# Performance work log

Hardware: AMD Instinct MI355X
Metric: run time of the kernel (lower is better)

## Reference

```python
import jax, jax.numpy as jnp
import numpy as np

B, L, D = 64, 128, 768          # batch, padded seq len, bert dim
H, HA = 1024, 256               # d_label_hidden, d_label_hidden_arc
POS, V = 18, 40                 # pos vocab, arc (deprel) vocab


def setup_inputs() -> dict:
    key = jax.random.key(0)
    ks = jax.random.split(key, 24)
    n = lambda i, shape, s=0.02: jax.random.normal(ks[i], shape, jnp.float32) * s
    # realistic padding: random sentence lengths in [L//2, L]
    lengths = jax.random.randint(ks[1], (B,), L // 2, L + 1)
    pad_mask = (jnp.arange(L)[None, :] < lengths[:, None]).astype(jnp.float32)
    heads = jax.random.randint(ks[2], (B, L), 0, L)
    # mark padded positions as -1 (zero head vector), as in the original loop
    heads = jnp.where(pad_mask > 0, heads, -1)
    return {
        "ann": jax.random.normal(ks[0], (B, L, D), jnp.float32),
        "pad_mask": pad_mask,
        "correct_heads": heads,
        # label-biaffine branch (hidden H)
        "W_head_mlp": n(3, (D, H)), "b_head_mlp": n(4, (H,)),
        "W_dep_mlp": n(5, (D, H)), "b_dep_mlp": n(6, (H,)),
        "W_lin": n(7, (H, H)), "b_lin": n(8, (H,)),
        "head_vec": n(9, (H,), 1.0), "dep_vec": n(10, (H,), 1.0),
        "bias": n(11, (1, 1, 1), 1.0),
        # arc-label biaffine branch (hidden HA, per-label bilinear)
        "W_head_arc_mlp": n(12, (D, HA)), "b_head_arc_mlp": n(13, (HA,)),
        "W_dep_arc_mlp": n(14, (D, HA)), "b_dep_arc_mlp": n(15, (HA,)),
        "W_arc": n(16, (V, HA, HA), 1.0),
        "head_vec_arc": n(17, (HA, V), 1.0), "dep_vec_arc": n(18, (HA, V), 1.0),
        "bias_arc": n(19, (1, 1, V), 1.0),
        # POS tip
        "W_pos": n(20, (D, POS)), "b_pos": n(21, (POS,)),
    }


def reference(ann, pad_mask, correct_heads,
              W_head_mlp, b_head_mlp, W_dep_mlp, b_dep_mlp,
              W_lin, b_lin, head_vec, dep_vec, bias,
              W_head_arc_mlp, b_head_arc_mlp, W_dep_arc_mlp, b_dep_arc_mlp,
              W_arc, head_vec_arc, dep_vec_arc, bias_arc,
              W_pos, b_pos):
    # POS prediction
    pos_pred = ann @ W_pos + b_pos                                  # [B,L,POS]

    # ---- dependency (unlabeled arc) biaffine ----
    ann_head = jax.nn.relu(ann @ W_head_mlp + b_head_mlp)           # [B,L,H]
    ann_dep = jax.nn.relu(ann @ W_dep_mlp + b_dep_mlp)              # [B,L,H]
    head_bias = ann_head @ head_vec                                 # [B,L]
    dep_bias = ann_dep @ dep_vec                                    # [B,L]
    Wh = ann_head @ W_lin + b_lin                                   # [B,L,H]
    # scores[b,i,j] = dep[b,i] . Wh[b,j]
    dep_W_headT = jnp.einsum('bih,bjh->bij', ann_dep, Wh)
    dep_W_headT = dep_W_headT + head_bias[:, None, :] + dep_bias[:, :, None] + bias
    valid_head = pad_mask[:, None, :] > 0                           # [B,1,L]
    dep_W_headT = jnp.where(valid_head, dep_W_headT, -jnp.inf)

    # ---- labeled arc biaffine (gather gold head per dependent) ----
    ann_head_arc = jax.nn.relu(ann @ W_head_arc_mlp + b_head_arc_mlp)  # [B,L,HA]
    ann_dep_arc = jax.nn.relu(ann @ W_dep_arc_mlp + b_dep_arc_mlp)     # [B,L,HA]
    idx = jnp.clip(correct_heads, 0, L - 1)
    gathered = jnp.take_along_axis(ann_head_arc, idx[:, :, None], axis=1)
    gathered = jnp.where((correct_heads == -1)[:, :, None], 0.0, gathered)  # [B,L,HA]

    head_arc_bias = gathered @ head_vec_arc                         # [B,L,V]
    dep_arc_bias = ann_dep_arc @ dep_vec_arc                        # [B,L,V]
    # per-label bilinear: s[b,l,v] = gathered[b,l] . W_arc[v] . dep[b,l]
    dep_W_headT_arc = jnp.einsum('bld,vde,ble->blv', gathered, W_arc, ann_dep_arc)
    dep_W_headT_arc = dep_W_headT_arc + head_arc_bias + dep_arc_bias + bias_arc

    return pos_pred, dep_W_headT, dep_W_headT_arc
```

## Files before the change

### kernel.cpp

```cpp
#include <hip/hip_runtime.h>
#include <hip/hip_bf16.h>

#define B_ 64
#define L_ 128
#define D_ 768
#define H_ 1024
#define HA_ 256
#define POS_ 18
#define V_ 40
#define BL_ (B_ * L_)

#define NEG_BIG (-1.0e30f)

typedef __attribute__((ext_vector_type(8))) short short8v;
typedef __attribute__((ext_vector_type(4))) short short4v;
typedef __attribute__((ext_vector_type(4))) float f32x4;

__device__ inline void split_bf16(float x, short& hi, short& lo) {
  __hip_bfloat16 h = __float2bfloat16(x);
  hi = *reinterpret_cast<short*>(&h);
  const float r = x - __bfloat162float(h);
  __hip_bfloat16 l = __float2bfloat16(r);
  lo = *reinterpret_cast<short*>(&l);
}

__device__ __forceinline__ short f2b(float x) {
  __hip_bfloat16 h = __float2bfloat16(x);
  return *reinterpret_cast<short*>(&h);
}
__device__ __forceinline__ float b2f(short s) {
  __hip_bfloat16 h = *reinterpret_cast<__hip_bfloat16*>(&s);
  return __bfloat162float(h);
}

__device__ __forceinline__ int swz8(int row, int s) { return ((s + (row >> 1)) & 3) * 8; }
__device__ __forceinline__ int colswz(int row, int n) {
  return (n & ~31) + swz8(row, (n >> 3) & 3) + (n & 7);
}

__device__ __forceinline__ void ld_lds16(const void* g, void* l) {
  __builtin_amdgcn_global_load_lds(
      (const __attribute__((address_space(1))) unsigned int*)g,
      (__attribute__((address_space(3))) unsigned int*)l, 16, 0, 0);
}

template<bool RELU, bool HASBIAS>
__global__ __launch_bounds__(256)
void gemm_bias(const float* __restrict__ A, const float* __restrict__ Bm,
               const float* __restrict__ bias, float* __restrict__ C,
               int M, int N, int K) {
  __shared__ __align__(16) float As[16][68];
  __shared__ __align__(16) float Bs[16][68];
  const int t = threadIdx.x;
  const int tx = t & 15, ty = t >> 4;
  const int m0 = blockIdx.y * 64, n0 = blockIdx.x * 64;
  const int arow = t >> 2, aks = (t & 3) * 4;
  const int bkr = t >> 4, bns = (t & 15) * 4;
  float acc[4][4] = {};
  for (int k0 = 0; k0 < K; k0 += 16) {
    const float4 av = *reinterpret_cast<const float4*>(&A[(size_t)(m0 + arow) * K + k0 + aks]);
    float4 bv;
    const int nb = n0 + bns;
    if (nb + 3 < N) {
      bv = *reinterpret_cast<const float4*>(&Bm[(size_t)(k0 + bkr) * N + nb]);
    } else {
      bv.x = (nb + 0 < N) ? Bm[(size_t)(k0 + bkr) * N + nb + 0] : 0.f;
      bv.y = (nb + 1 < N) ? Bm[(size_t)(k0 + bkr) * N + nb + 1] : 0.f;
      bv.z = (nb + 2 < N) ? Bm[(size_t)(k0 + bkr) * N + nb + 2] : 0.f;
      bv.w = 0.f;
    }
    __syncthreads();
    As[aks + 0][arow] = av.x;
    As[aks + 1][arow] = av.y;
    As[aks + 2][arow] = av.z;
    As[aks + 3][arow] = av.w;
    *reinterpret_cast<float4*>(&Bs[bkr][bns]) = bv;
    __syncthreads();
#pragma unroll
    for (int kk = 0; kk < 16; ++kk) {
      const float4 a4 = *reinterpret_cast<const float4*>(&As[kk][ty * 4]);
      const float4 b4 = *reinterpret_cast<const float4*>(&Bs[kk][tx * 4]);
      const float aa[4] = {a4.x, a4.y, a4.z, a4.w};
      const float bb[4] = {b4.x, b4.y, b4.z, b4.w};
#pragma unroll
      for (int i = 0; i < 4; ++i)
#pragma unroll
        for (int j = 0; j < 4; ++j)
          acc[i][j] = fmaf(aa[i], bb[j], acc[i][j]);
    }
  }
#pragma unroll
  for (int j = 0; j < 4; ++j) {
    const int n = n0 + tx * 4 + j;
    if (n >= N) continue;
    float bj = 0.f;
    if constexpr (HASBIAS) bj = bias[n];
#pragma unroll
    for (int i = 0; i < 4; ++i) {
      const int m = m0 + ty * 4 + i;
      float v = acc[i][j] + bj;
      if (RELU) v = fmaxf(v, 0.f);
      C[(size_t)m * N + n] = v;
    }
  }
}

__global__ __launch_bounds__(256)
void split_pre(const float* __restrict__ src, short* __restrict__ hi,
               short* __restrict__ lo, int K) {
  const int t = threadIdx.x;
  const int r = blockIdx.x * 4 + (t >> 6);
  const int lane = t & 63;
  for (int c = lane * 4; c < K; c += 256) {
    const float4 v = *reinterpret_cast<const float4*>(&src[(size_t)r * K + c]);
    const float vv[4] = {v.x, v.y, v.z, v.w};
    short4v h4, l4;
#pragma unroll
    for (int j = 0; j < 4; ++j) {
      short h, l;
      split_bf16(vv[j], h, l);
      h4[j] = h; l4[j] = l;
    }
    const int cs = colswz(r, c);
    *reinterpret_cast<short4v*>(&hi[(size_t)r * K + cs]) = h4;
    *reinterpret_cast<short4v*>(&lo[(size_t)r * K + cs]) = l4;
  }
}

__global__ __launch_bounds__(256)
void transpose_h(const float* __restrict__ W, short* __restrict__ Thi,
                 int K, int N) {
  __shared__ float tile[32][33];
  const int k0 = blockIdx.y * 32, n0 = blockIdx.x * 32;
  const int t = threadIdx.x;
  const int r = t >> 3, c = (t & 7) * 4;
  const float4 w4 = *reinterpret_cast<const float4*>(&W[(size_t)(k0 + r) * N + n0 + c]);
  tile[r][c + 0] = w4.x;
  tile[r][c + 1] = w4.y;
  tile[r][c + 2] = w4.z;
  tile[r][c + 3] = w4.w;
  __syncthreads();
  short4v hi4;
#pragma unroll
  for (int j = 0; j < 4; ++j) hi4[j] = f2b(tile[c + j][r]);
  const int row = n0 + r;
  const int cs = swz8(row, (c >> 3) & 3) + (c & 7);
  *reinterpret_cast<short4v*>(&Thi[(size_t)row * K + k0 + cs]) = hi4;
}

__global__ __launch_bounds__(256)
void transpose_pos(const float* __restrict__ W, short* __restrict__ Th,
                   short* __restrict__ Tl) {
  const int t = threadIdx.x;
  const int k0 = blockIdx.x * 32;
  const int n = t & 31;
  const int ks = (t >> 5) * 4;
#pragma unroll
  for (int j = 0; j < 4; ++j) {
    const int k = k0 + ks + j;
    const float v = (n < POS_) ? W[(size_t)k * POS_ + n] : 0.f;
    short h, l;
    split_bf16(v, h, l);
    Th[(size_t)n * D_ + colswz(n, k)] = h;
    Tl[(size_t)n * D_ + colswz(n, k)] = l;
  }
}

#define GEMM_H_BODY                                                           \
  __shared__ __align__(16) short AhP[2][4096];                                \
  __shared__ __align__(16) short BhP[2][4096];                                \
  const int t = threadIdx.x;                                                  \
  const int lane = t & 63, w = t >> 6;                                        \
  const int wm = w >> 1, wn = w & 1;                                          \
  const int m0 = blockIdx.y * 128, n0 = blockIdx.x * 128;                     \
  const int fr = lane & 15, kgi = lane >> 4;                                  \
  const int drow = lane >> 2, dslot = lane & 3;                               \
  f32x4 acc[4][4] = {};                                                       \
  const int nt = K >> 5;                                                      \
  auto stage = [&](int tt, int pb) {                  \
    const int k0 = tt << 5;                                                   \
    _Pragma("unroll")                                                         \
    for (int cc = 0; cc < 2; ++cc) {                                          \
      const int c = w * 2 + cc;                                               \
      const size_t ga = (size_t)(m0 + c * 16 + drow) * K + k0 + dslot * 8;    \
      ld_lds16(&Ath[ga], &AhP[pb][c * 512]);                                  \
      const size_t gb = (size_t)(n0 + c * 16 + drow) * K + k0 + dslot * 8;    \
      ld_lds16(&Bth[gb], &BhP[pb][c * 512]);                                  \
    }                                                                         \
  };                                                                          \
  auto compute = [&](int pb) {                                                \
    short8v ah[4];                                                            \
    _Pragma("unroll")                                                         \
    for (int mi = 0; mi < 4; ++mi) {                                          \
      const int r = wm * 64 + mi * 16 + fr;                                   \
      ah[mi] = *reinterpret_cast<const short8v*>(&AhP[pb][r * 32 + swz8(r, kgi)]); \
    }                                                                         \
    __builtin_amdgcn_s_setprio(1);                                            \
    _Pragma("unroll")                                                         \
    for (int nj = 0; nj < 4; ++nj) {                                          \
      const int rn = wn * 64 + nj * 16 + fr;                                  \
      const short8v bh = *reinterpret_cast<const short8v*>(&BhP[pb][rn * 32 + swz8(rn, kgi)]); \
      _Pragma("unroll")                                                       \
      for (int mi = 0; mi < 4; ++mi)                                          \
        acc[mi][nj] = __builtin_amdgcn_mfma_f32_16x16x32_bf16(ah[mi], bh, acc[mi][nj], 0, 0, 0); \
    }                                                                         \
    __builtin_amdgcn_s_setprio(0);                                            \
  };                                                                          \
  stage(0, 0);                                                                \
  int cur = 0;                                                                \
  for (int tt = 0; tt < nt; ++tt) {                                           \
    if (tt + 1 < nt) {                                                        \
      stage(tt + 1, cur ^ 1);                                                 \
      asm volatile("s_waitcnt vmcnt(4)" ::: "memory");                        \
    } else {                                                                  \
      asm volatile("s_waitcnt vmcnt(0)" ::: "memory");                        \
    }                                                                         \
    __builtin_amdgcn_s_barrier();                                             \
    compute(cur);                                                             \
    __builtin_amdgcn_s_barrier();                                             \
    cur ^= 1;                                                                 \
  }                                                                           \
  const int rg = lane >> 4;

template<bool RELU>
__global__ __launch_bounds__(256)
void gemm_h(const short* __restrict__ Ath, const short* __restrict__ Bth,
            const float* __restrict__ bias, float* __restrict__ C,
            int M, int N, int K) {
  GEMM_H_BODY
#pragma unroll
  for (int nj = 0; nj < 4; ++nj) {
    const int n = n0 + wn * 64 + nj * 16 + fr;
    const float bj = bias[n];
#pragma unroll
    for (int mi = 0; mi < 4; ++mi) {
#pragma unroll
      for (int q = 0; q < 4; ++q) {
        const int m = m0 + wm * 64 + mi * 16 + rg * 4 + q;
        float v2 = acc[mi][nj][q] + bj;
        if (RELU) v2 = fmaxf(v2, 0.f);
        C[(size_t)m * N + n] = v2;
      }
    }
  }
}

template<bool RELU>
__global__ __launch_bounds__(256)
void gemm_hs(const short* __restrict__ Ath, const short* __restrict__ Bth,
             const float* __restrict__ bias, short* __restrict__ Oh,
             int M, int N, int K) {
  GEMM_H_BODY
#pragma unroll
  for (int nj = 0; nj < 4; ++nj) {
    const int n = n0 + wn * 64 + nj * 16 + fr;
    const float bj = bias[n];
#pragma unroll
    for (int mi = 0; mi < 4; ++mi) {
#pragma unroll
      for (int q = 0; q < 4; ++q) {
        const int m = m0 + wm * 64 + mi * 16 + rg * 4 + q;
        float v2 = acc[mi][nj][q] + bj;
        if (RELU) v2 = fmaxf(v2, 0.f);
        Oh[(size_t)m * N + colswz(m, n)] = f2b(v2);
      }
    }
  }
}

__global__ __launch_bounds__(256)
void pos_mfma(const short* __restrict__ Ath, const short* __restrict__ Atl,
              const short* __restrict__ Pth, const short* __restrict__ Ptl,
              const float* __restrict__ bias, float* __restrict__ out) {
  extern __shared__ short sm[];
  short* AhP = sm;
  short* AlP = sm + 16384;
  short* BhP = sm + 32768;
  short* BlP = sm + 34816;
  const int t = threadIdx.x;
  const int m0 = blockIdx.x * 256;
  const int lane = t & 63, w = t >> 6;
  const int fr = lane & 15, kgi = lane >> 4;
  const int drow = lane >> 2, dslot = lane & 3;
  f32x4 acc[4][2] = {};

  auto stage = [&](int tt, int pb) {
    const int k0 = tt << 5;
#pragma unroll
    for (int cc = 0; cc < 4; ++cc) {
      const int c = w * 4 + cc;
      const size_t ga = (size_t)(m0 + c * 16 + drow) * D_ + k0 + dslot * 8;
      ld_lds16(&Ath[ga], &AhP[pb * 8192 + c * 512]);
      ld_lds16(&Atl[ga], &AlP[pb * 8192 + c * 512]);
    }
    {
      const short* bsrc = (w & 2) ? Ptl : Pth;
      short* bdst = (w & 2) ? BlP : BhP;
      const int c = w & 1;
      const size_t gb = (size_t)(c * 16 + drow) * D_ + k0 + dslot * 8;
      ld_lds16(&bsrc[gb], &bdst[pb * 1024 + c * 512]);
    }
  };
  auto compute = [&](int pb) {
    short8v ah[4], al[4];
#pragma unroll
    for (int mi = 0; mi < 4; ++mi) {
      const int r = w * 64 + mi * 16 + fr;
      const int sw = swz8(r, kgi);
      ah[mi] = *reinterpret_cast<const short8v*>(&AhP[pb * 8192 + r * 32 + sw]);
      al[mi] = *reinterpret_cast<const short8v*>(&AlP[pb * 8192 + r * 32 + sw]);
    }
#pragma unroll
    for (int nj = 0; nj < 2; ++nj) {
      const int rn = nj * 16 + fr;
      const int sw = swz8(rn, kgi);
      const short8v bh = *reinterpret_cast<const short8v*>(&BhP[pb * 1024 + rn * 32 + sw]);
      const short8v bl = *reinterpret_cast<const short8v*>(&BlP[pb * 1024 + rn * 32 + sw]);
#pragma unroll
      for (int mi = 0; mi < 4; ++mi) {
        acc[mi][nj] = __builtin_amdgcn_mfma_f32_16x16x32_bf16(ah[mi], bh, acc[mi][nj], 0, 0, 0);
        acc[mi][nj] = __builtin_amdgcn_mfma_f32_16x16x32_bf16(al[mi], bh, acc[mi][nj], 0, 0, 0);
        acc[mi][nj] = __builtin_amdgcn_mfma_f32_16x16x32_bf16(ah[mi], bl, acc[mi][nj], 0, 0, 0);
      }
    }
  };

  stage(0, 0);
  __syncthreads();
  int cur = 0;
  for (int tt = 0; tt < 24; ++tt) {
    if (tt + 1 < 24) stage(tt + 1, cur ^ 1);
    compute(cur);
    __syncthreads();
    cur ^= 1;
  }

  const int rg = lane >> 4;
#pragma unroll
  for (int nj = 0; nj < 2; ++nj) {
    const int n = nj * 16 + fr;
    if (n >= POS_) continue;
    const float bj = bias[n];
#pragma unroll
    for (int mi = 0; mi < 4; ++mi) {
#pragma unroll
      for (int q = 0; q < 4; ++q) {
        const int m = m0 + w * 64 + mi * 16 + rg * 4 + q;
        out[(size_t)m * POS_ + n] = acc[mi][nj][q] + bj;
      }
    }
  }
}

__global__ __launch_bounds__(256)
void bias_dots_h(const short* __restrict__ Ahh, const short* __restrict__ Adh,
                 const float* __restrict__ head_vec, const float* __restrict__ dep_vec,
                 float* __restrict__ hb, float* __restrict__ db) {
  const int m = blockIdx.x;
  const int t = threadIdx.x;
  const int c = t * 4;
  const size_t o = (size_t)m * H_ + colswz(m, c);
  const short4v h4 = *reinterpret_cast<const short4v*>(&Ahh[o]);
  const short4v d4 = *reinterpret_cast<const short4v*>(&Adh[o]);
  const float4 hv = *reinterpret_cast<const float4*>(&head_vec[c]);
  const float4 dv = *reinterpret_cast<const float4*>(&dep_vec[c]);
  const float hvv[4] = {hv.x, hv.y, hv.z, hv.w};
  const float dvv[4] = {dv.x, dv.y, dv.z, dv.w};
  float sh = 0.f, sd = 0.f;
#pragma unroll
  for (int j = 0; j < 4; ++j) {
    sh = fmaf(b2f(h4[j]), hvv[j], sh);
    sd = fmaf(b2f(d4[j]), dvv[j], sd);
  }
#pragma unroll
  for (int off = 32; off; off >>= 1) {
    sh += __shfl_xor(sh, off);
    sd += __shfl_xor(sd, off);
  }
  __shared__ float redh[4], redd[4];
  const int w = t >> 6;
  if ((t & 63) == 0) { redh[w] = sh; redd[w] = sd; }
  __syncthreads();
  if (t == 0) {
    hb[m] = redh[0] + redh[1] + redh[2] + redh[3];
    db[m] = redd[0] + redd[1] + redd[2] + redd[3];
  }
}

__global__ __launch_bounds__(256)
void scores_h(const short* __restrict__ Adh, const short* __restrict__ Whh,
              const float* __restrict__ hb, const float* __restrict__ db,
              const float* __restrict__ pad_mask, const float* __restrict__ bias1,
              float* __restrict__ out2) {
  __shared__ __align__(16) short AhP[2][2048];
  __shared__ __align__(16) short BhP[2][2048];
  const int t = threadIdx.x;
  const int b = blockIdx.z;
  const int i0 = blockIdx.y * 64, j0 = blockIdx.x * 64;
  const int lane = t & 63, w = t >> 6;
  const int wm = w >> 1, wn = w & 1;
  const int fr = lane & 15, kgi = lane >> 4;
  const int drow = lane >> 2, dslot = lane & 3;
  const size_t abase = ((size_t)b * L_ + i0) * H_;
  const size_t bbase = ((size_t)b * L_ + j0) * H_;
  f32x4 acc[2][2] = {};

  auto stage = [&](int tt, int pb) {
    const int k0 = tt << 5;
    const size_t ga = abase + (size_t)(w * 16 + drow) * H_ + k0 + dslot * 8;
    ld_lds16(&Adh[ga], &AhP[pb][w * 512]);
    const size_t gb = bbase + (size_t)(w * 16 + drow) * H_ + k0 + dslot * 8;
    ld_lds16(&Whh[gb], &BhP[pb][w * 512]);
  };
  auto compute = [&](int pb) {
    short8v ah[2];
#pragma unroll
    for (int mi = 0; mi < 2; ++mi) {
      const int r = wm * 32 + mi * 16 + fr;
      ah[mi] = *reinterpret_cast<const short8v*>(&AhP[pb][r * 32 + swz8(r, kgi)]);
    }
    __builtin_amdgcn_s_setprio(1);
#pragma unroll
    for (int nj = 0; nj < 2; ++nj) {
      const int rn = wn * 32 + nj * 16 + fr;
      const short8v bh = *reinterpret_cast<const short8v*>(&BhP[pb][rn * 32 + swz8(rn, kgi)]);
#pragma unroll
      for (int mi = 0; mi < 2; ++mi)
        acc[mi][nj] = __builtin_amdgcn_mfma_f32_16x16x32_bf16(ah[mi], bh, acc[mi][nj], 0, 0, 0);
    }
    __builtin_amdgcn_s_setprio(0);
  };

  stage(0, 0);
  int cur = 0;
  for (int tt = 0; tt < 32; ++tt) {
    if (tt + 1 < 32) {
      stage(tt + 1, cur ^ 1);
      asm volatile("s_waitcnt vmcnt(2)" ::: "memory");
    } else {
      asm volatile("s_waitcnt vmcnt(0)" ::: "memory");
    }
    __builtin_amdgcn_s_barrier();
    compute(cur);
    __builtin_amdgcn_s_barrier();
    cur ^= 1;
  }

  const int rg = lane >> 4;
  const float bias0 = bias1[0];
#pragma unroll
  for (int nj = 0; nj < 2; ++nj) {
    const int jcol = j0 + wn * 32 + nj * 16 + fr;
    const float mj = pad_mask[b * L_ + jcol];
    const float hbj = hb[b * L_ + jcol];
#pragma unroll
    for (int mi = 0; mi < 2; ++mi) {
#pragma unroll
      for (int q = 0; q < 4; ++q) {
        const int irow = i0 + wm * 32 + mi * 16 + rg * 4 + q;
        float v = acc[mi][nj][q] + hbj + db[b * L_ + irow] + bias0;
        if (!(mj > 0.f)) v = NEG_BIG;
        out2[((size_t)b * L_ + irow) * L_ + jcol] = v;
      }
    }
  }
}

__global__ __launch_bounds__(256)
void transposeW_h(const float* __restrict__ W, short* __restrict__ Whi) {
  __shared__ float tile[32][33];
  const int v = blockIdx.z, d0 = blockIdx.y * 32, e0 = blockIdx.x * 32;
  const int t = threadIdx.x;
  const int r = t >> 3, c = (t & 7) * 4;
  const float4 w4 = *reinterpret_cast<const float4*>(
      &W[((size_t)v * HA_ + d0 + r) * HA_ + e0 + c]);
  tile[r][c + 0] = w4.x;
  tile[r][c + 1] = w4.y;
  tile[r][c + 2] = w4.z;
  tile[r][c + 3] = w4.w;
  __syncthreads();
  short4v hi4;
#pragma unroll
  for (int j = 0; j < 4; ++j) hi4[j] = f2b(tile[c + j][r]);
  const int row = e0 + r;
  const int cs = swz8(row, (c >> 3) & 3) + (c & 7);
  *reinterpret_cast<short4v*>(&Whi[((size_t)v * HA_ + row) * HA_ + d0 + cs]) = hi4;
}

__global__ __launch_bounds__(256)
void gather_h(const float* __restrict__ head_arcb, const int* __restrict__ heads,
              float* __restrict__ g32, short* __restrict__ g_hi) {
  const int t = threadIdx.x;
  const int m = blockIdx.x * 4 + (t >> 6);
  const int lane = t & 63;
  const int h = heads[m];
  float4 g4 = make_float4(0.f, 0.f, 0.f, 0.f);
  if (h >= 0)
    g4 = *reinterpret_cast<const float4*>(
        &head_arcb[((size_t)((m >> 7) * L_ + h)) * HA_ + lane * 4]);
  *reinterpret_cast<float4*>(&g32[(size_t)m * HA_ + lane * 4]) = g4;
  short4v hi4;
  const float gv[4] = {g4.x, g4.y, g4.z, g4.w};
#pragma unroll
  for (int j = 0; j < 4; ++j) hi4[j] = f2b(gv[j]);
  *reinterpret_cast<short4v*>(&g_hi[(size_t)m * HA_ + colswz(m, lane * 4)]) = hi4;
}

__global__ __launch_bounds__(512)
void arc_h(const short* __restrict__ g_hi, const short* __restrict__ Wt_hi,
           const float* __restrict__ dep32, const float* __restrict__ hb_arc,
           const float* __restrict__ db_arc, float* __restrict__ out3) {
  extern __shared__ short sm[];
  short* AhP = sm;
  short* BhP = sm + 16384;
  __shared__ float parts[256][2];
  const int t = threadIdx.x;
  const int bid = blockIdx.x;
  const int xcd = bid & 7;
  const int j = bid >> 3;
  const int m0 = (j / 5) * 256;
  const int v = xcd * 5 + (j % 5);
  const int lane = t & 63, w = t >> 6;
  const int wm = w >> 1, we = w & 1;
  const int fr = lane & 15, kgi = lane >> 4;
  const int drow = lane >> 2, dslot = lane & 3;
  const size_t wbase = (size_t)v * HA_ * HA_;

  f32x4 acc[4][8] = {};

  auto stage = [&](int tt, int pb) {
    const int k0 = tt << 5;
#pragma unroll
    for (int cc = 0; cc < 2; ++cc) {
      const int c = w * 2 + cc;
      const size_t ga = (size_t)(m0 + c * 16 + drow) * HA_ + k0 + dslot * 8;
      ld_lds16(&g_hi[ga], &AhP[pb * 8192 + c * 512]);
      const size_t gb = wbase + (size_t)(c * 16 + drow) * HA_ + k0 + dslot * 8;
      ld_lds16(&Wt_hi[gb], &BhP[pb * 8192 + c * 512]);
    }
  };
  auto compute = [&](int pb) {
    short8v ah[4];
#pragma unroll
    for (int mi = 0; mi < 4; ++mi) {
      const int r = wm * 64 + mi * 16 + fr;
      ah[mi] = *reinterpret_cast<const short8v*>(&AhP[pb * 8192 + r * 32 + swz8(r, kgi)]);
    }
    __builtin_amdgcn_s_setprio(1);
#pragma unroll
    for (int ej = 0; ej < 8; ++ej) {
      const int rb = we * 128 + ej * 16 + fr;
      const short8v bh = *reinterpret_cast<const short8v*>(&BhP[pb * 8192 + rb * 32 + swz8(rb, kgi)]);
#pragma unroll
      for (int mi = 0; mi < 4; ++mi)
        acc[mi][ej] = __builtin_amdgcn_mfma_f32_16x16x32_bf16(ah[mi], bh, acc[mi][ej], 0, 0, 0);
    }
    __builtin_amdgcn_s_setprio(0);
  };

  stage(0, 0);
  int cur = 0;
#pragma unroll
  for (int tt = 0; tt < 8; ++tt) {
    if (tt < 7) {
      stage(tt + 1, cur ^ 1);
      asm volatile("s_waitcnt vmcnt(4)" ::: "memory");
    } else {
      asm volatile("s_waitcnt vmcnt(0)" ::: "memory");
    }
    __builtin_amdgcn_s_barrier();
    compute(cur);
    __builtin_amdgcn_s_barrier();
    cur ^= 1;
  }

  const int rg = lane >> 4;
#pragma unroll
  for (int mi = 0; mi < 4; ++mi) {
#pragma unroll
    for (int q = 0; q < 4; ++q) {
      const int mrow = wm * 64 + mi * 16 + rg * 4 + q;
      const int m = m0 + mrow;
      float s = 0.f;
#pragma unroll
      for (int ej = 0; ej < 8; ++ej)
        s = fmaf(acc[mi][ej][q], dep32[(size_t)m * HA_ + we * 128 + ej * 16 + fr], s);
      s += __shfl_xor(s, 1, 16);
      s += __shfl_xor(s, 2, 16);
      s += __shfl_xor(s, 4, 16);
      s += __shfl_xor(s, 8, 16);
      if (fr == 0) parts[mrow][we] = s;
    }
  }
  __syncthreads();
  if (t < 256) {
    const int m = m0 + t;
    out3[(size_t)m * V_ + v] =
        parts[t][0] + parts[t][1] + hb_arc[(size_t)m * V_ + v] + db_arc[(size_t)m * V_ + v];
  }
}

extern "C" void kernel_launch(void* const* d_in, const int* in_sizes, int n_in,
                              void* d_out, int out_size, void* d_ws, size_t ws_size,
                              hipStream_t stream) {
  const float* ann        = (const float*)d_in[0];
  const float* pad_mask   = (const float*)d_in[1];
  const int*   heads      = (const int*)d_in[2];
  const float* W_head_mlp = (const float*)d_in[3];
  const float* b_head_mlp = (const float*)d_in[4];
  const float* W_dep_mlp  = (const float*)d_in[5];
  const float* b_dep_mlp  = (const float*)d_in[6];
  const float* W_lin      = (const float*)d_in[7];
  const float* b_lin      = (const float*)d_in[8];
  const float* head_vec   = (const float*)d_in[9];
  const float* dep_vec    = (const float*)d_in[10];
  const float* bias1      = (const float*)d_in[11];
  const float* W_head_arc = (const float*)d_in[12];
  const float* b_head_arc = (const float*)d_in[13];
  const float* W_dep_arc  = (const float*)d_in[14];
  const float* b_dep_arc  = (const float*)d_in[15];
  const float* W_arc      = (const float*)d_in[16];
  const float* hv_arc     = (const float*)d_in[17];
  const float* dv_arc     = (const float*)d_in[18];
  const float* bias_arc   = (const float*)d_in[19];
  const float* W_pos      = (const float*)d_in[20];
  const float* b_pos      = (const float*)d_in[21];

  float* out_pos    = (float*)d_out;
  float* out_scores = out_pos + (size_t)BL_ * POS_;
  float* out_arc    = out_scores + (size_t)B_ * L_ * L_;

  float* ws  = (float*)d_ws;
  float* R1  = ws;
  float* R2  = R1 + (size_t)BL_ * H_;
  float* R3  = R2 + (size_t)BL_ * H_;
  float* head_arcb = R3 + (size_t)BL_ * H_;
  float* dep_arcb  = head_arcb + (size_t)BL_ * HA_;
  float* hb        = dep_arcb + (size_t)BL_ * HA_;
  float* db        = hb + BL_;
  short* wt0     = (short*)(db + BL_);
  short* Wth_hm  = wt0;
  short* Wth_dm  = Wth_hm + (size_t)H_ * D_;
  short* Wth_lin = Wth_dm + (size_t)H_ * D_;
  short* Wth_ha  = Wth_lin + (size_t)H_ * H_;
  short* Wth_da  = Wth_ha + (size_t)HA_ * D_;
  short* Pth     = Wth_da + (size_t)HA_ * D_;
  short* Ptl     = Pth + (size_t)32 * D_;
  short* Ahh = (short*)R1;
  short* Adh = (short*)R2;
  short* Ath = (short*)R3;  short* Atl = Ath + (size_t)BL_ * D_;
  short* Whh = (short*)R3;
  float* g32 = (float*)wt0;
  short* Wt_hi  = (short*)R1;
  short* g_hi   = Wt_hi + (size_t)V_ * HA_ * HA_;
  float* hb_arc = (float*)(g_hi + (size_t)BL_ * HA_);
  float* db_arc = hb_arc + (size_t)BL_ * V_;

  {
    hipFuncSetAttribute((const void*)pos_mfma, hipFuncAttributeMaxDynamicSharedMemorySize, 73728);
    hipFuncSetAttribute((const void*)arc_h, hipFuncAttributeMaxDynamicSharedMemorySize, 65536);
  }

  const dim3 blk(256);
  split_pre<<<dim3(BL_ / 4), blk, 0, stream>>>(ann, Ath, Atl, D_);
  transpose_h<<<dim3(H_ / 32, D_ / 32), blk, 0, stream>>>(W_head_mlp, Wth_hm, D_, H_);
  transpose_h<<<dim3(H_ / 32, D_ / 32), blk, 0, stream>>>(W_dep_mlp, Wth_dm, D_, H_);
  transpose_h<<<dim3(H_ / 32, H_ / 32), blk, 0, stream>>>(W_lin, Wth_lin, H_, H_);
  transpose_h<<<dim3(HA_ / 32, D_ / 32), blk, 0, stream>>>(W_head_arc, Wth_ha, D_, HA_);
  transpose_h<<<dim3(HA_ / 32, D_ / 32), blk, 0, stream>>>(W_dep_arc, Wth_da, D_, HA_);
  transpose_pos<<<dim3(D_ / 32), blk, 0, stream>>>(W_pos, Pth, Ptl);

  gemm_hs<true><<<dim3(H_ / 128, BL_ / 128), blk, 0, stream>>>(
      Ath, Wth_hm, b_head_mlp, Ahh, BL_, H_, D_);
  gemm_hs<true><<<dim3(H_ / 128, BL_ / 128), blk, 0, stream>>>(
      Ath, Wth_dm, b_dep_mlp, Adh, BL_, H_, D_);
  gemm_h<true><<<dim3(HA_ / 128, BL_ / 128), blk, 0, stream>>>(
      Ath, Wth_ha, b_head_arc, head_arcb, BL_, HA_, D_);
  gemm_h<true><<<dim3(HA_ / 128, BL_ / 128), blk, 0, stream>>>(
      Ath, Wth_da, b_dep_arc, dep_arcb, BL_, HA_, D_);
  pos_mfma<<<dim3(BL_ / 256), blk, 73728, stream>>>(Ath, Atl, Pth, Ptl, b_pos, out_pos);
  gemm_hs<false><<<dim3(H_ / 128, BL_ / 128), blk, 0, stream>>>(
      Ahh, Wth_lin, b_lin, Whh, BL_, H_, H_);

  bias_dots_h<<<dim3(BL_), blk, 0, stream>>>(Ahh, Adh, head_vec, dep_vec, hb, db);
  scores_h<<<dim3(2, 2, B_), blk, 0, stream>>>(
      Adh, Whh, hb, db, pad_mask, bias1, out_scores);

  transposeW_h<<<dim3(HA_ / 32, HA_ / 32, V_), blk, 0, stream>>>(W_arc, Wt_hi);
  gather_h<<<dim3(BL_ / 4), blk, 0, stream>>>(head_arcb, heads, g32, g_hi);
  gemm_bias<false, true><<<dim3(1, BL_ / 64), blk, 0, stream>>>(
      g32, hv_arc, bias_arc, hb_arc, BL_, V_, HA_);
  gemm_bias<false, false><<<dim3(1, BL_ / 64), blk, 0, stream>>>(
      dep_arcb, dv_arc, nullptr, db_arc, BL_, V_, HA_);
  arc_h<<<dim3((BL_ / 256) * V_), dim3(512), 65536, stream>>>(
      g_hi, Wt_hi, dep_arcb, hb_arc, db_arc, out_arc);
}
```

Before: 302.0 us.

## Fuse dep-arc bias into arc kernel, retile arc_h, restructure bias dots and pos sync

The dep_arc_bias GEMM is folded into the arc bilinear kernel: dv_arc[e,v] is added to each accumulator before the dot with the dep vector, which removes one launch and the db_arc round trip. arc_h drops from 512 to 256 threads with 128-row tiles and static LDS, doubling the grid. bias_dots_h now computes one row per wavefront with no shared-memory reduction, and pos_mfma replaces __syncthreads with explicit vmcnt waits plus raw barriers. The vmcnt counts are hand-tuned and depend on how many loads each stage issues.

```diff
diff --git a/kernel.cpp b/kernel.cpp
--- a/kernel.cpp
+++ b/kernel.cpp
@@ -326,12 +326,17 @@
   };
 
   stage(0, 0);
-  __syncthreads();
   int cur = 0;
   for (int tt = 0; tt < 24; ++tt) {
-    if (tt + 1 < 24) stage(tt + 1, cur ^ 1);
+    if (tt + 1 < 24) {
+      stage(tt + 1, cur ^ 1);
+      asm volatile("s_waitcnt vmcnt(9)" ::: "memory");
+    } else {
+      asm volatile("s_waitcnt vmcnt(0)" ::: "memory");
+    }
+    __builtin_amdgcn_s_barrier();
     compute(cur);
-    __syncthreads();
+    __builtin_amdgcn_s_barrier();
     cur ^= 1;
   }
 
@@ -356,34 +361,34 @@
 void bias_dots_h(const short* __restrict__ Ahh, const short* __restrict__ Adh,
                  const float* __restrict__ head_vec, const float* __restrict__ dep_vec,
                  float* __restrict__ hb, float* __restrict__ db) {
-  const int m = blockIdx.x;
-  const int t = threadIdx.x;
-  const int c = t * 4;
-  const size_t o = (size_t)m * H_ + colswz(m, c);
-  const short4v h4 = *reinterpret_cast<const short4v*>(&Ahh[o]);
-  const short4v d4 = *reinterpret_cast<const short4v*>(&Adh[o]);
-  const float4 hv = *reinterpret_cast<const float4*>(&head_vec[c]);
-  const float4 dv = *reinterpret_cast<const float4*>(&dep_vec[c]);
-  const float hvv[4] = {hv.x, hv.y, hv.z, hv.w};
-  const float dvv[4] = {dv.x, dv.y, dv.z, dv.w};
+  const int t = threadIdx.x;
+  const int m = blockIdx.x * 4 + (t >> 6);
+  const int lane = t & 63;
   float sh = 0.f, sd = 0.f;
 #pragma unroll
-  for (int j = 0; j < 4; ++j) {
-    sh = fmaf(b2f(h4[j]), hvv[j], sh);
-    sd = fmaf(b2f(d4[j]), dvv[j], sd);
+  for (int jj = 0; jj < 4; ++jj) {
+    const int c = lane * 16 + jj * 4;
+    const size_t o = (size_t)m * H_ + colswz(m, c);
+    const short4v h4 = *reinterpret_cast<const short4v*>(&Ahh[o]);
+    const short4v d4 = *reinterpret_cast<const short4v*>(&Adh[o]);
+    const float4 hv = *reinterpret_cast<const float4*>(&head_vec[c]);
+    const float4 dv = *reinterpret_cast<const float4*>(&dep_vec[c]);
+    const float hvv[4] = {hv.x, hv.y, hv.z, hv.w};
+    const float dvv[4] = {dv.x, dv.y, dv.z, dv.w};
+#pragma unroll
+    for (int j = 0; j < 4; ++j) {
+      sh = fmaf(b2f(h4[j]), hvv[j], sh);
+      sd = fmaf(b2f(d4[j]), dvv[j], sd);
+    }
   }
 #pragma unroll
   for (int off = 32; off; off >>= 1) {
     sh += __shfl_xor(sh, off);
     sd += __shfl_xor(sd, off);
   }
-  __shared__ float redh[4], redd[4];
-  const int w = t >> 6;
-  if ((t & 63) == 0) { redh[w] = sh; redd[w] = sd; }
-  __syncthreads();
-  if (t == 0) {
-    hb[m] = redh[0] + redh[1] + redh[2] + redh[3];
-    db[m] = redd[0] + redd[1] + redd[2] + redd[3];
+  if (lane == 0) {
+    hb[m] = sh;
+    db[m] = sd;
   }
 }
 
@@ -506,19 +511,18 @@
   *reinterpret_cast<short4v*>(&g_hi[(size_t)m * HA_ + colswz(m, lane * 4)]) = hi4;
 }
 
-__global__ __launch_bounds__(512)
+__global__ __launch_bounds__(256)
 void arc_h(const short* __restrict__ g_hi, const short* __restrict__ Wt_hi,
            const float* __restrict__ dep32, const float* __restrict__ hb_arc,
-           const float* __restrict__ db_arc, float* __restrict__ out3) {
-  extern __shared__ short sm[];
-  short* AhP = sm;
-  short* BhP = sm + 16384;
-  __shared__ float parts[256][2];
+           const float* __restrict__ dv_arc, float* __restrict__ out3) {
+  __shared__ __align__(16) short AhP[2][4096];
+  __shared__ __align__(16) short BhP[2][8192];
+  __shared__ float parts[128][2];
   const int t = threadIdx.x;
   const int bid = blockIdx.x;
   const int xcd = bid & 7;
   const int j = bid >> 3;
-  const int m0 = (j / 5) * 256;
+  const int m0 = (j / 5) * 128;
   const int v = xcd * 5 + (j % 5);
   const int lane = t & 63, w = t >> 6;
   const int wm = w >> 1, we = w & 1;
@@ -534,9 +538,13 @@
     for (int cc = 0; cc < 2; ++cc) {
       const int c = w * 2 + cc;
       const size_t ga = (size_t)(m0 + c * 16 + drow) * HA_ + k0 + dslot * 8;
-      ld_lds16(&g_hi[ga], &AhP[pb * 8192 + c * 512]);
+      ld_lds16(&g_hi[ga], &AhP[pb][c * 512]);
+    }
+#pragma unroll
+    for (int cc = 0; cc < 4; ++cc) {
+      const int c = w * 4 + cc;
       const size_t gb = wbase + (size_t)(c * 16 + drow) * HA_ + k0 + dslot * 8;
-      ld_lds16(&Wt_hi[gb], &BhP[pb * 8192 + c * 512]);
+      ld_lds16(&Wt_hi[gb], &BhP[pb][c * 512]);
     }
   };
   auto compute = [&](int pb) {
@@ -544,13 +552,13 @@
 #pragma unroll
     for (int mi = 0; mi < 4; ++mi) {
       const int r = wm * 64 + mi * 16 + fr;
-      ah[mi] = *reinterpret_cast<const short8v*>(&AhP[pb * 8192 + r * 32 + swz8(r, kgi)]);
+      ah[mi] = *reinterpret_cast<const short8v*>(&AhP[pb][r * 32 + swz8(r, kgi)]);
     }
     __builtin_amdgcn_s_setprio(1);
 #pragma unroll
     for (int ej = 0; ej < 8; ++ej) {
       const int rb = we * 128 + ej * 16 + fr;
-      const short8v bh = *reinterpret_cast<const short8v*>(&BhP[pb * 8192 + rb * 32 + swz8(rb, kgi)]);
+      const short8v bh = *reinterpret_cast<const short8v*>(&BhP[pb][rb * 32 + swz8(rb, kgi)]);
 #pragma unroll
       for (int mi = 0; mi < 4; ++mi)
         acc[mi][ej] = __builtin_amdgcn_mfma_f32_16x16x32_bf16(ah[mi], bh, acc[mi][ej], 0, 0, 0);
@@ -564,7 +572,7 @@
   for (int tt = 0; tt < 8; ++tt) {
     if (tt < 7) {
       stage(tt + 1, cur ^ 1);
-      asm volatile("s_waitcnt vmcnt(4)" ::: "memory");
+      asm volatile("s_waitcnt vmcnt(6)" ::: "memory");
     } else {
       asm volatile("s_waitcnt vmcnt(0)" ::: "memory");
     }
@@ -575,6 +583,10 @@
   }
 
   const int rg = lane >> 4;
+  float dvr[8];
+#pragma unroll
+  for (int ej = 0; ej < 8; ++ej)
+    dvr[ej] = dv_arc[(size_t)(we * 128 + ej * 16 + fr) * V_ + v];
 #pragma unroll
   for (int mi = 0; mi < 4; ++mi) {
 #pragma unroll
@@ -584,7 +596,8 @@
       float s = 0.f;
 #pragma unroll
       for (int ej = 0; ej < 8; ++ej)
-        s = fmaf(acc[mi][ej][q], dep32[(size_t)m * HA_ + we * 128 + ej * 16 + fr], s);
+        s = fmaf(acc[mi][ej][q] + dvr[ej],
+                 dep32[(size_t)m * HA_ + we * 128 + ej * 16 + fr], s);
       s += __shfl_xor(s, 1, 16);
       s += __shfl_xor(s, 2, 16);
       s += __shfl_xor(s, 4, 16);
@@ -593,10 +606,9 @@
     }
   }
   __syncthreads();
-  if (t < 256) {
+  if (t < 128) {
     const int m = m0 + t;
-    out3[(size_t)m * V_ + v] =
-        parts[t][0] + parts[t][1] + hb_arc[(size_t)m * V_ + v] + db_arc[(size_t)m * V_ + v];
+    out3[(size_t)m * V_ + v] = parts[t][0] + parts[t][1] + hb_arc[(size_t)m * V_ + v];
   }
 }
 
@@ -654,12 +666,8 @@
   short* Wt_hi  = (short*)R1;
   short* g_hi   = Wt_hi + (size_t)V_ * HA_ * HA_;
   float* hb_arc = (float*)(g_hi + (size_t)BL_ * HA_);
-  float* db_arc = hb_arc + (size_t)BL_ * V_;
-
-  {
-    hipFuncSetAttribute((const void*)pos_mfma, hipFuncAttributeMaxDynamicSharedMemorySize, 73728);
-    hipFuncSetAttribute((const void*)arc_h, hipFuncAttributeMaxDynamicSharedMemorySize, 65536);
-  }
+
+  hipFuncSetAttribute((const void*)pos_mfma, hipFuncAttributeMaxDynamicSharedMemorySize, 73728);
 
   const dim3 blk(256);
   split_pre<<<dim3(BL_ / 4), blk, 0, stream>>>(ann, Ath, Atl, D_);
@@ -682,7 +690,7 @@
   gemm_hs<false><<<dim3(H_ / 128, BL_ / 128), blk, 0, stream>>>(
       Ahh, Wth_lin, b_lin, Whh, BL_, H_, H_);
 
-  bias_dots_h<<<dim3(BL_), blk, 0, stream>>>(Ahh, Adh, head_vec, dep_vec, hb, db);
+  bias_dots_h<<<dim3(BL_ / 4), blk, 0, stream>>>(Ahh, Adh, head_vec, dep_vec, hb, db);
   scores_h<<<dim3(2, 2, B_), blk, 0, stream>>>(
       Adh, Whh, hb, db, pad_mask, bias1, out_scores);
 
@@ -690,8 +698,6 @@
   gather_h<<<dim3(BL_ / 4), blk, 0, stream>>>(head_arcb, heads, g32, g_hi);
   gemm_bias<false, true><<<dim3(1, BL_ / 64), blk, 0, stream>>>(
       g32, hv_arc, bias_arc, hb_arc, BL_, V_, HA_);
-  gemm_bias<false, false><<<dim3(1, BL_ / 64), blk, 0, stream>>>(
-      dep_arcb, dv_arc, nullptr, db_arc, BL_, V_, HA_);
-  arc_h<<<dim3((BL_ / 256) * V_), dim3(512), 65536, stream>>>(
-      g_hi, Wt_hi, dep_arcb, hb_arc, db_arc, out_arc);
-}
+  arc_h<<<dim3((BL_ / 128) * V_), blk, 0, stream>>>(
+      g_hi, Wt_hi, dep_arcb, hb_arc, dv_arc, out_arc);
+}
```

New measurement: 291.6 us. 1.04x faster.
